# Kernel optimization log

Measured on AMD Instinct MI355X. Metric: run time of the kernel, lower is better.

Reference implementation:

```python
import jax, jax.numpy as jnp
import numpy as np

# Inside algorithm for a binary TreeCRF over a complete binary tree in heap
# layout: node i has children 2i+1 and 2i+2; level of size n starts at index
# n-1. Leaves are the last (n_nodes+1)//2 entries of `emissions`.
#
# Original per-node math:
#   inside[p] = logsumexp_{i,j}( em[p] + trans[p,i] + left[i] + trans[p,j] + right[j] )
# which factorizes exactly as
#   inside[p] = em[p] + logsumexp_i(trans[p,i]+left[i]) + logsumexp_j(trans[p,j]+right[j])


def setup_inputs() -> dict:
    key = jax.random.key(0)
    k1, k2 = jax.random.split(key)
    n_leaves = 131072  # 2**17
    n_nodes = 2 * n_leaves - 1  # 262143
    L = 32
    emissions = jax.random.normal(k1, (n_nodes, L), dtype=jnp.float32)
    trans = jax.random.normal(k2, (L, L), dtype=jnp.float32)
    return {"emissions": emissions, "trans": trans}


def _child_contrib(trans, child):
    # child: [n, L] inside scores of children; trans: [L, L]
    # returns [n, L]: logsumexp_c(trans[p, c] + child[:, c])
    return jax.nn.logsumexp(trans[None, :, :] + child[:, None, :], axis=2)


def reference(emissions, trans):
    n_nodes = emissions.shape[0]
    n_leaves = (n_nodes + 1) // 2
    # leaf inside scores are just the leaf emissions
    scores = emissions[n_leaves - 1:]  # [n_leaves, L]
    level = n_leaves // 2
    while level >= 1:
        # children of node (level-1)+k are scores[2k] (left) and scores[2k+1] (right)
        left = scores[0::2]   # [level, L]
        right = scores[1::2]  # [level, L]
        em = emissions[level - 1: 2 * level - 1]  # [level, L]
        scores = em + _child_contrib(trans, left) + _child_contrib(trans, right)
        level //= 2
    return scores[0]  # root inside score, [L]
```

## Files before the change

### kernel.cpp

```cpp
#include <hip/hip_runtime.h>


typedef float f32x4 __attribute__((ext_vector_type(4)));
typedef short s16x8 __attribute__((ext_vector_type(8)));
typedef short s16x4 __attribute__((ext_vector_type(4)));

__device__ __forceinline__ short f2bf(float f) {
    unsigned u = __builtin_bit_cast(unsigned, f);
    unsigned r = (u + 0x7fffu + ((u >> 16) & 1u)) >> 16;
    return (short)r;
}

#define MSTEP(mask) { float4 o; o.x=__shfl_xor(r.x,mask); o.y=__shfl_xor(r.y,mask); \
                      o.z=__shfl_xor(r.z,mask); o.w=__shfl_xor(r.w,mask); \
                      r.x=fmaxf(r.x,o.x); r.y=fmaxf(r.y,o.y); \
                      r.z=fmaxf(r.z,o.z); r.w=fmaxf(r.w,o.w); }

template <int NT, int LEVELS>
__device__ __forceinline__ void run_tree(
    const int t, int Wp, int boff, const int b,
    const float* __restrict__ gchild,
    const float* __restrict__ em,
    const s16x8 a0, const s16x8 a1,
    short* __restrict__ CA, float* __restrict__ MA,
    short* __restrict__ CB, float* __restrict__ MB,
    float* __restrict__ gout)
{
    const int NC0 = 1 << LEVELS;
    for (int u = t; u < NC0 * 8; u += NT) {
        int ql = u >> 3, k = u & 7;
        float4 x = ((const float4*)(gchild + (size_t)ql * 32))[k];
        float4 r = x;
        MSTEP(1) MSTEP(2) MSTEP(4)
        float m = fmaxf(fmaxf(r.x, r.y), fmaxf(r.z, r.w));
        s16x4 w;
        w[0] = f2bf(__expf(x.x - m)); w[1] = f2bf(__expf(x.y - m));
        w[2] = f2bf(__expf(x.z - m)); w[3] = f2bf(__expf(x.w - m));
        *((s16x4*)(CA + ql * 32 + k * 4)) = w;
        if (k == 0) MA[ql] = m;
    }
    __syncthreads();

    short* Cs = CA; float* Ms = MA;
    short* Cd = CB; float* Md = MB;
    const int lane = t & 63, wv = t >> 6, nw = NT / 64;
    const int ql = lane & 15, kg = lane >> 4;
    int nc = NC0;
    for (int l = 0; l < LEVELS; ++l) {
        int nqt = (nc >= 16) ? (nc >> 4) : 1;
        for (int qt = wv; qt < nqt; qt += nw) {
            int q = qt * 16 + ql;
            bool valid = q < nc;
            s16x8 bf = *((const s16x8*)(Cs + q * 32 + kg * 8));
            f32x4 d0 = {0.f, 0.f, 0.f, 0.f};
            f32x4 d1 = {0.f, 0.f, 0.f, 0.f};
            d0 = __builtin_amdgcn_mfma_f32_16x16x32_bf16(a0, bf, d0, 0, 0, 0);
            d1 = __builtin_amdgcn_mfma_f32_16x16x32_bf16(a1, bf, d1, 0, 0, 0);
            float mq = Ms[q];
            int p = qt * 8 + (ql >> 1);
            size_t node = (size_t)(Wp - 1) + (size_t)boff * b + p;
            const float4 e0 = *((const float4*)(em + node * 32 + kg * 4));
            const float4 e1 = *((const float4*)(em + node * 32 + 16 + kg * 4));
            float v0[4], v1[4];
#pragma unroll
            for (int r2 = 0; r2 < 4; ++r2) {
                float t0 = mq + __logf(d0[r2]);
                float t1 = mq + __logf(d1[r2]);
                v0[r2] = t0 + __shfl_xor(t0, 1);
                v1[r2] = t1 + __shfl_xor(t1, 1);
            }
            v0[0] += e0.x; v0[1] += e0.y; v0[2] += e0.z; v0[3] += e0.w;
            v1[0] += e1.x; v1[1] += e1.y; v1[2] += e1.z; v1[3] += e1.w;
            if (l == LEVELS - 1) {
                if (ql == 0) {
                    float4 o0 = {v0[0], v0[1], v0[2], v0[3]};
                    float4 o1 = {v1[0], v1[1], v1[2], v1[3]};
                    *((float4*)(gout + kg * 4)) = o0;
                    *((float4*)(gout + 16 + kg * 4)) = o1;
                }
            } else {
                float m2 = fmaxf(fmaxf(fmaxf(v0[0], v0[1]), fmaxf(v0[2], v0[3])),
                                 fmaxf(fmaxf(v1[0], v1[1]), fmaxf(v1[2], v1[3])));
                m2 = fmaxf(m2, __shfl_xor(m2, 16));
                m2 = fmaxf(m2, __shfl_xor(m2, 32));
                if (valid && !(ql & 1)) {
                    s16x4 w0, w1;
                    w0[0] = f2bf(__expf(v0[0] - m2)); w0[1] = f2bf(__expf(v0[1] - m2));
                    w0[2] = f2bf(__expf(v0[2] - m2)); w0[3] = f2bf(__expf(v0[3] - m2));
                    w1[0] = f2bf(__expf(v1[0] - m2)); w1[1] = f2bf(__expf(v1[1] - m2));
                    w1[2] = f2bf(__expf(v1[2] - m2)); w1[3] = f2bf(__expf(v1[3] - m2));
                    *((s16x4*)(Cd + p * 32 + kg * 4)) = w0;
                    *((s16x4*)(Cd + p * 32 + 16 + kg * 4)) = w1;
                    if (kg == 0) Md[p] = m2;
                }
            }
        }
        __syncthreads();
        short* tc = Cs; Cs = Cd; Cd = tc;
        float* tm = Ms; Ms = Md; Md = tm;
        nc >>= 1; Wp >>= 1; boff >>= 1;
    }
}

__device__ __forceinline__ void load_afrag(const float* __restrict__ trans,
                                           int row, int kg, s16x8* a)
{
#pragma unroll
    for (int j = 0; j < 8; ++j)
        (*a)[j] = f2bf(__expf(trans[row * 32 + kg * 8 + j]));
}

__global__ __launch_bounds__(512) void treecrf_fused(
    const float* __restrict__ em, const float* __restrict__ trans,
    float* __restrict__ out512, int* __restrict__ counter,
    float* __restrict__ out_root, int n_leaves, int nbm1)
{
    __shared__ short CA[512 * 32];
    __shared__ short CB[256 * 32];
    __shared__ float MA[512];
    __shared__ float MB[256];
    __shared__ int last_flag;
    int t = threadIdx.x, b = blockIdx.x;
    int ql = t & 15, kg = (t & 63) >> 4;
    s16x8 a0, a1;
    load_afrag(trans, ql, kg, &a0);
    load_afrag(trans, ql + 16, kg, &a1);

    run_tree<512, 8>(t, n_leaves >> 1, 128, b,
                     em + (size_t)(n_leaves - 1 + 256 * b) * 32, em, a0, a1,
                     CA, MA, CB, MB, out512 + (size_t)b * 32);

    if (t == 0) {
        __threadfence();
        last_flag = (atomicAdd(counter, 1) == nbm1);
    }
    __syncthreads();
    if (!last_flag) return;
    __threadfence();

    run_tree<512, 9>(t, 256, 0, 0, out512, em, a0, a1,
                     CA, MA, CB, MB, out_root);
}

extern "C" void kernel_launch(void* const* d_in, const int* in_sizes, int n_in,
                              void* d_out, int out_size, void* d_ws, size_t ws_size,
                              hipStream_t stream)
{
    const float* em = (const float*)d_in[0];
    const float* trans = (const float*)d_in[1];
    int n_nodes = in_sizes[0] / 32;
    int n_leaves = (n_nodes + 1) / 2;
    int blocks = n_leaves / 256;

    float* out512 = (float*)d_ws;
    int* counter = (int*)((char*)d_ws + 512 * 32 * sizeof(float));

    hipMemsetAsync(counter, 0, sizeof(int), stream);
    treecrf_fused<<<dim3(blocks), dim3(512), 0, stream>>>(
        em, trans, out512, counter, (float*)d_out, n_leaves, blocks - 1);
}
```

Measured before the change: 109.7 us.

## Split tree reduction into per-wave 32-leaf subtrees across three launches

Replaces the single fused kernel, which used 512-thread blocks over 256-leaf subtrees and a last-block atomic counter, with three launches. Each wave independently reduces a 32-node subtree through five levels, so block-wide barriers that used to cover many idle waves at the upper levels are gone. Shared rows are padded to a stride of 40 to reduce LDS bank conflicts. The cost is extra kernel launches and extra workspace round trips, and the middle stage runs only 32 blocks.

```diff
diff --git a/kernel.cpp b/kernel.cpp
--- a/kernel.cpp
+++ b/kernel.cpp
@@ -5,101 +5,16 @@
 typedef short s16x8 __attribute__((ext_vector_type(8)));
 typedef short s16x4 __attribute__((ext_vector_type(4)));
 
+#define CSTR 40
+
 __device__ __forceinline__ short f2bf(float f) {
     unsigned u = __builtin_bit_cast(unsigned, f);
     unsigned r = (u + 0x7fffu + ((u >> 16) & 1u)) >> 16;
     return (short)r;
 }
 
-#define MSTEP(mask) { float4 o; o.x=__shfl_xor(r.x,mask); o.y=__shfl_xor(r.y,mask); \
-                      o.z=__shfl_xor(r.z,mask); o.w=__shfl_xor(r.w,mask); \
-                      r.x=fmaxf(r.x,o.x); r.y=fmaxf(r.y,o.y); \
-                      r.z=fmaxf(r.z,o.z); r.w=fmaxf(r.w,o.w); }
-
-template <int NT, int LEVELS>
-__device__ __forceinline__ void run_tree(
-    const int t, int Wp, int boff, const int b,
-    const float* __restrict__ gchild,
-    const float* __restrict__ em,
-    const s16x8 a0, const s16x8 a1,
-    short* __restrict__ CA, float* __restrict__ MA,
-    short* __restrict__ CB, float* __restrict__ MB,
-    float* __restrict__ gout)
-{
-    const int NC0 = 1 << LEVELS;
-    for (int u = t; u < NC0 * 8; u += NT) {
-        int ql = u >> 3, k = u & 7;
-        float4 x = ((const float4*)(gchild + (size_t)ql * 32))[k];
-        float4 r = x;
-        MSTEP(1) MSTEP(2) MSTEP(4)
-        float m = fmaxf(fmaxf(r.x, r.y), fmaxf(r.z, r.w));
-        s16x4 w;
-        w[0] = f2bf(__expf(x.x - m)); w[1] = f2bf(__expf(x.y - m));
-        w[2] = f2bf(__expf(x.z - m)); w[3] = f2bf(__expf(x.w - m));
-        *((s16x4*)(CA + ql * 32 + k * 4)) = w;
-        if (k == 0) MA[ql] = m;
-    }
-    __syncthreads();
-
-    short* Cs = CA; float* Ms = MA;
-    short* Cd = CB; float* Md = MB;
-    const int lane = t & 63, wv = t >> 6, nw = NT / 64;
-    const int ql = lane & 15, kg = lane >> 4;
-    int nc = NC0;
-    for (int l = 0; l < LEVELS; ++l) {
-        int nqt = (nc >= 16) ? (nc >> 4) : 1;
-        for (int qt = wv; qt < nqt; qt += nw) {
-            int q = qt * 16 + ql;
-            bool valid = q < nc;
-            s16x8 bf = *((const s16x8*)(Cs + q * 32 + kg * 8));
-            f32x4 d0 = {0.f, 0.f, 0.f, 0.f};
-            f32x4 d1 = {0.f, 0.f, 0.f, 0.f};
-            d0 = __builtin_amdgcn_mfma_f32_16x16x32_bf16(a0, bf, d0, 0, 0, 0);
-            d1 = __builtin_amdgcn_mfma_f32_16x16x32_bf16(a1, bf, d1, 0, 0, 0);
-            float mq = Ms[q];
-            int p = qt * 8 + (ql >> 1);
-            size_t node = (size_t)(Wp - 1) + (size_t)boff * b + p;
-            const float4 e0 = *((const float4*)(em + node * 32 + kg * 4));
-            const float4 e1 = *((const float4*)(em + node * 32 + 16 + kg * 4));
-            float v0[4], v1[4];
-#pragma unroll
-            for (int r2 = 0; r2 < 4; ++r2) {
-                float t0 = mq + __logf(d0[r2]);
-                float t1 = mq + __logf(d1[r2]);
-                v0[r2] = t0 + __shfl_xor(t0, 1);
-                v1[r2] = t1 + __shfl_xor(t1, 1);
-            }
-            v0[0] += e0.x; v0[1] += e0.y; v0[2] += e0.z; v0[3] += e0.w;
-            v1[0] += e1.x; v1[1] += e1.y; v1[2] += e1.z; v1[3] += e1.w;
-            if (l == LEVELS - 1) {
-                if (ql == 0) {
-                    float4 o0 = {v0[0], v0[1], v0[2], v0[3]};
-                    float4 o1 = {v1[0], v1[1], v1[2], v1[3]};
-                    *((float4*)(gout + kg * 4)) = o0;
-                    *((float4*)(gout + 16 + kg * 4)) = o1;
-                }
-            } else {
-                float m2 = fmaxf(fmaxf(fmaxf(v0[0], v0[1]), fmaxf(v0[2], v0[3])),
-                                 fmaxf(fmaxf(v1[0], v1[1]), fmaxf(v1[2], v1[3])));
-                m2 = fmaxf(m2, __shfl_xor(m2, 16));
-                m2 = fmaxf(m2, __shfl_xor(m2, 32));
-                if (valid && !(ql & 1)) {
-                    s16x4 w0, w1;
-                    w0[0] = f2bf(__expf(v0[0] - m2)); w0[1] = f2bf(__expf(v0[1] - m2));
-                    w0[2] = f2bf(__expf(v0[2] - m2)); w0[3] = f2bf(__expf(v0[3] - m2));
-                    w1[0] = f2bf(__expf(v1[0] - m2)); w1[1] = f2bf(__expf(v1[1] - m2));
-                    w1[2] = f2bf(__expf(v1[2] - m2)); w1[3] = f2bf(__expf(v1[3] - m2));
-                    *((s16x4*)(Cd + p * 32 + kg * 4)) = w0;
-                    *((s16x4*)(Cd + p * 32 + 16 + kg * 4)) = w1;
-                    if (kg == 0) Md[p] = m2;
-                }
-            }
-        }
-        __syncthreads();
-        short* tc = Cs; Cs = Cd; Cd = tc;
-        float* tm = Ms; Ms = Md; Md = tm;
-        nc >>= 1; Wp >>= 1; boff >>= 1;
-    }
+__device__ __forceinline__ float max4(float4 v) {
+    return fmaxf(fmaxf(v.x, v.y), fmaxf(v.z, v.w));
 }
 
 __device__ __forceinline__ void load_afrag(const float* __restrict__ trans,
@@ -110,36 +25,132 @@
         (*a)[j] = f2bf(__expf(trans[row * 32 + kg * 8 + j]));
 }
 
-__global__ __launch_bounds__(512) void treecrf_fused(
-    const float* __restrict__ em, const float* __restrict__ trans,
-    float* __restrict__ out512, int* __restrict__ counter,
-    float* __restrict__ out_root, int n_leaves, int nbm1)
+template <int NC0>
+__device__ __forceinline__ void wave_reduce(
+    bool active, int lane,
+    const float* rows, const float* __restrict__ em, int inW, int sid,
+    s16x8 a0, s16x8 a1, short* C, float* M, float* outrow)
 {
-    __shared__ short CA[512 * 32];
-    __shared__ short CB[256 * 32];
-    __shared__ float MA[512];
-    __shared__ float MB[256];
-    __shared__ int last_flag;
-    int t = threadIdx.x, b = blockIdx.x;
-    int ql = t & 15, kg = (t & 63) >> 4;
-    s16x8 a0, a1;
-    load_afrag(trans, ql, kg, &a0);
-    load_afrag(trans, ql + 16, kg, &a1);
-
-    run_tree<512, 8>(t, n_leaves >> 1, 128, b,
-                     em + (size_t)(n_leaves - 1 + 256 * b) * 32, em, a0, a1,
-                     CA, MA, CB, MB, out512 + (size_t)b * 32);
-
-    if (t == 0) {
-        __threadfence();
-        last_flag = (atomicAdd(counter, 1) == nbm1);
+    constexpr int STEPS = (NC0 == 32) ? 5 : 2;
+    if (active) {
+        int q = lane & 31, h = lane >> 5;
+        if (q < NC0) {
+            const float4* src = (const float4*)(rows + q * 32 + h * 16);
+            float4 x0 = src[0], x1 = src[1], x2 = src[2], x3 = src[3];
+            float mm = fmaxf(fmaxf(max4(x0), max4(x1)),
+                             fmaxf(max4(x2), max4(x3)));
+            mm = fmaxf(mm, __shfl_xor(mm, 32));
+            s16x8 w0, w1;
+            w0[0] = f2bf(__expf(x0.x - mm)); w0[1] = f2bf(__expf(x0.y - mm));
+            w0[2] = f2bf(__expf(x0.z - mm)); w0[3] = f2bf(__expf(x0.w - mm));
+            w0[4] = f2bf(__expf(x1.x - mm)); w0[5] = f2bf(__expf(x1.y - mm));
+            w0[6] = f2bf(__expf(x1.z - mm)); w0[7] = f2bf(__expf(x1.w - mm));
+            w1[0] = f2bf(__expf(x2.x - mm)); w1[1] = f2bf(__expf(x2.y - mm));
+            w1[2] = f2bf(__expf(x2.z - mm)); w1[3] = f2bf(__expf(x2.w - mm));
+            w1[4] = f2bf(__expf(x3.x - mm)); w1[5] = f2bf(__expf(x3.y - mm));
+            w1[6] = f2bf(__expf(x3.z - mm)); w1[7] = f2bf(__expf(x3.w - mm));
+            *(s16x8*)(C + q * CSTR + h * 16) = w0;
+            *(s16x8*)(C + q * CSTR + h * 16 + 8) = w1;
+            if (h == 0) M[q] = mm;
+        }
     }
     __syncthreads();
-    if (!last_flag) return;
-    __threadfence();
+    const int ql = lane & 15, kg = lane >> 4;
+    int nc = NC0;
+#pragma unroll
+    for (int s = 1; s <= STEPS; ++s) {
+        const int Wp = inW >> s;
+        const int nstr = (nc + 15) >> 4;
+        for (int st = 0; st < nstr; ++st) {
+            if (active) {
+                int q = st * 16 + ql;
+                bool valid = q < nc;
+                s16x8 b = *(const s16x8*)(C + q * CSTR + kg * 8);
+                f32x4 d0 = {0.f, 0.f, 0.f, 0.f};
+                f32x4 d1 = {0.f, 0.f, 0.f, 0.f};
+                d0 = __builtin_amdgcn_mfma_f32_16x16x32_bf16(a0, b, d0, 0, 0, 0);
+                d1 = __builtin_amdgcn_mfma_f32_16x16x32_bf16(a1, b, d1, 0, 0, 0);
+                float mq = M[q];
+                int p = q >> 1;
+                size_t node = (size_t)(Wp - 1) + (size_t)sid * (NC0 >> s) + p;
+                float4 e0 = *((const float4*)(em + node * 32 + kg * 4));
+                float4 e1 = *((const float4*)(em + node * 32 + 16 + kg * 4));
+                float v0[4], v1[4];
+#pragma unroll
+                for (int r = 0; r < 4; ++r) {
+                    float t0 = mq + __logf(d0[r]);
+                    float t1 = mq + __logf(d1[r]);
+                    v0[r] = t0 + __shfl_xor(t0, 1);
+                    v1[r] = t1 + __shfl_xor(t1, 1);
+                }
+                v0[0] += e0.x; v0[1] += e0.y; v0[2] += e0.z; v0[3] += e0.w;
+                v1[0] += e1.x; v1[1] += e1.y; v1[2] += e1.z; v1[3] += e1.w;
+                if (s == STEPS) {
+                    if (ql == 0) {
+                        float4 o0 = {v0[0], v0[1], v0[2], v0[3]};
+                        float4 o1 = {v1[0], v1[1], v1[2], v1[3]};
+                        *(float4*)(outrow + kg * 4) = o0;
+                        *(float4*)(outrow + 16 + kg * 4) = o1;
+                    }
+                } else {
+                    float m2 = fmaxf(
+                        fmaxf(fmaxf(v0[0], v0[1]), fmaxf(v0[2], v0[3])),
+                        fmaxf(fmaxf(v1[0], v1[1]), fmaxf(v1[2], v1[3])));
+                    m2 = fmaxf(m2, __shfl_xor(m2, 16));
+                    m2 = fmaxf(m2, __shfl_xor(m2, 32));
+                    if (valid && !(q & 1)) {
+                        s16x4 u0, u1;
+                        u0[0] = f2bf(__expf(v0[0] - m2));
+                        u0[1] = f2bf(__expf(v0[1] - m2));
+                        u0[2] = f2bf(__expf(v0[2] - m2));
+                        u0[3] = f2bf(__expf(v0[3] - m2));
+                        u1[0] = f2bf(__expf(v1[0] - m2));
+                        u1[1] = f2bf(__expf(v1[1] - m2));
+                        u1[2] = f2bf(__expf(v1[2] - m2));
+                        u1[3] = f2bf(__expf(v1[3] - m2));
+                        *(s16x4*)(C + p * CSTR + kg * 4) = u0;
+                        *(s16x4*)(C + p * CSTR + 16 + kg * 4) = u1;
+                        if (kg == 0) M[p] = m2;
+                    }
+                }
+            }
+        }
+        __syncthreads();
+        nc >>= 1;
+    }
+}
 
-    run_tree<512, 9>(t, 256, 0, 0, out512, em, a0, a1,
-                     CA, MA, CB, MB, out_root);
+__global__ __launch_bounds__(256) void treecrf_stage(
+    const float* __restrict__ rows_base, const float* __restrict__ em,
+    const float* __restrict__ trans, float* __restrict__ out, int inW)
+{
+    __shared__ short C[4 * 32 * CSTR];
+    __shared__ float M[4 * 32];
+    int t = threadIdx.x, lane = t & 63, wv = t >> 6;
+    int sid = blockIdx.x * 4 + wv;
+    s16x8 a0, a1;
+    load_afrag(trans, lane & 15, lane >> 4, &a0);
+    load_afrag(trans, (lane & 15) + 16, lane >> 4, &a1);
+    wave_reduce<32>(true, lane, rows_base + (size_t)sid * 1024, em, inW, sid,
+                    a0, a1, C + wv * 32 * CSTR, M + wv * 32,
+                    out + (size_t)sid * 32);
+}
+
+__global__ __launch_bounds__(256) void treecrf_final(
+    const float* __restrict__ ws2, const float* __restrict__ em,
+    const float* __restrict__ trans, float* __restrict__ out_root)
+{
+    __shared__ short C[4 * 32 * CSTR];
+    __shared__ float M[4 * 32];
+    __shared__ float R4[4 * 32];
+    int t = threadIdx.x, lane = t & 63, wv = t >> 6;
+    s16x8 a0, a1;
+    load_afrag(trans, lane & 15, lane >> 4, &a0);
+    load_afrag(trans, (lane & 15) + 16, lane >> 4, &a1);
+    wave_reduce<32>(true, lane, ws2 + (size_t)wv * 1024, em, 128, wv,
+                    a0, a1, C + wv * 32 * CSTR, M + wv * 32, R4 + wv * 32);
+    __syncthreads();
+    wave_reduce<4>(wv == 0, lane, R4, em, 4, 0, a0, a1, C, M, out_root);
 }
 
 extern "C" void kernel_launch(void* const* d_in, const int* in_sizes, int n_in,
@@ -150,12 +161,14 @@
     const float* trans = (const float*)d_in[1];
     int n_nodes = in_sizes[0] / 32;
     int n_leaves = (n_nodes + 1) / 2;
-    int blocks = n_leaves / 256;
 
-    float* out512 = (float*)d_ws;
-    int* counter = (int*)((char*)d_ws + 512 * 32 * sizeof(float));
+    float* ws1 = (float*)d_ws;
+    float* ws2 = ws1 + (size_t)4096 * 32;
 
-    hipMemsetAsync(counter, 0, sizeof(int), stream);
-    treecrf_fused<<<dim3(blocks), dim3(512), 0, stream>>>(
-        em, trans, out512, counter, (float*)d_out, n_leaves, blocks - 1);
+    treecrf_stage<<<dim3(n_leaves / 128), dim3(256), 0, stream>>>(
+        em + (size_t)(n_leaves - 1) * 32, em, trans, ws1, n_leaves);
+    treecrf_stage<<<dim3(32), dim3(256), 0, stream>>>(
+        ws1, em, trans, ws2, 4096);
+    treecrf_final<<<dim3(1), dim3(256), 0, stream>>>(
+        ws2, em, trans, (float*)d_out);
 }
```

Measured after the change: 98.04 us. 10.6% less time.
